# Kernel optimization log

Hardware: AMD Instinct MI355X
Metric: run time of the kernel (lower is better)

The kernel has to match this reference:

```python
import jax, jax.numpy as jnp
import numpy as np

HIDDEN = 2048
HEADS = 16
HEAD_DIM = HIDDEN // HEADS  # 128
ROPE_BASE = 10000.0
RMS_EPS = 1e-6
MINUS_INF = -10000.0


def rms_norm(x, w):
    xf = x.astype(jnp.float32)
    var = jnp.mean(xf * xf, axis=-1, keepdims=True)
    return w * (x * jax.lax.rsqrt(var + RMS_EPS))


def rotate_half(x):
    x1, x2 = jnp.split(x, 2, axis=-1)
    return jnp.concatenate((-x2, x1), axis=-1)


def rope_tables(seq_len, dtype):
    inv_freq = 1.0 / (ROPE_BASE ** (jnp.arange(0, HEAD_DIM, 2, dtype=jnp.float32) / HEAD_DIM))
    t = jnp.arange(seq_len, dtype=jnp.float32)
    freqs = jnp.einsum('i,j->ij', t, inv_freq)           # [S, D/2]
    emb = jnp.concatenate((freqs, freqs), axis=-1)       # [S, D]
    return jnp.cos(emb).astype(dtype), jnp.sin(emb).astype(dtype)


def setup_inputs() -> dict:
    key = jax.random.key(0)
    ks = jax.random.split(key, 6)
    B, S, H = 2, 2048, HIDDEN
    x = jax.random.normal(ks[0], (B, S, H), dtype=jnp.float32) * 0.5
    norm_w = jnp.ones((H,), dtype=jnp.float32)
    scale = 0.02
    wq = jax.random.normal(ks[1], (H, H), dtype=jnp.float32) * scale
    wk = jax.random.normal(ks[2], (H, H), dtype=jnp.float32) * scale
    wv = jax.random.normal(ks[3], (H, H), dtype=jnp.float32) * scale
    wo = jax.random.normal(ks[4], (H, H), dtype=jnp.float32) * scale
    position_ids = jnp.broadcast_to(jnp.arange(S, dtype=jnp.int32), (B, S))
    return {"x": x, "norm_w": norm_w, "wq": wq, "wk": wk, "wv": wv,
            "wo": wo, "position_ids": position_ids}


def reference(x, norm_w, wq, wk, wv, wo, position_ids):
    B, S, H = x.shape
    h = rms_norm(x, norm_w)
    # torch Linear: y = h @ W.T, weight is [out, in]
    def proj(w):
        return jnp.einsum('bsd,od->bso', h, w).reshape(B, S, HEADS, HEAD_DIM).transpose(0, 2, 1, 3)
    q, k, v = proj(wq), proj(wk), proj(wv)  # [B, Hh, S, D]
    cos, sin = rope_tables(S, x.dtype)
    cos = cos[position_ids][:, None]  # [B, 1, S, D]
    sin = sin[position_ids][:, None]
    q = q * cos + rotate_half(q) * sin
    k = k * cos + rotate_half(k) * sin
    scores = jnp.einsum('bhqd,bhkd->bhqk', q, k) / jnp.sqrt(jnp.float32(HEAD_DIM))
    causal = jnp.tril(jnp.ones((S, S), dtype=bool))
    scores = scores + jnp.where(causal, 0.0, MINUS_INF).astype(scores.dtype)
    probs = jax.nn.softmax(scores, axis=-1)
    ctx = jnp.einsum('bhqk,bhkd->bhqd', probs, v)          # [B, Hh, S, D]
    ctx = ctx.transpose(0, 2, 1, 3).reshape(B, S, H)
    out = jnp.einsum('bsd,od->bso', ctx, wo)
    return out
```

## Files before the change

### kernel.cpp

```cpp
#include <hip/hip_runtime.h>
#include <hip/hip_bf16.h>
#include <stdint.h>

#define S_LEN   2048
#define BATCH   2
#define HID     2048
#define NHEADS  16
#define HDIM    128
#define ROWS    (BATCH * S_LEN)
#define QKS     4096
#define ATT_SCALE 0.08838834764831843f
#define LOG2E     1.4426950408889634f

typedef __attribute__((ext_vector_type(8))) short s16x8;
typedef __attribute__((ext_vector_type(4))) float f32x4;

#define GLL16(gp, lp)                                                          \
  __builtin_amdgcn_global_load_lds(                                            \
      (__attribute__((address_space(1))) void*)(gp),                           \
      (__attribute__((address_space(3))) void*)(lp), 16, 0, 0)

__device__ __forceinline__ float bf2f(unsigned short u) {
  union { unsigned int i; float f; } v; v.i = ((unsigned int)u) << 16; return v.f;
}
__device__ __forceinline__ unsigned short f2bf(float f) {
  union { float f; unsigned int i; } v; v.f = f;
  unsigned int i = v.i;
  return (unsigned short)((i + 0x7FFFu + ((i >> 16) & 1u)) >> 16);
}
__device__ __forceinline__ void store_out(unsigned short* p, float v) { *p = f2bf(v); }
__device__ __forceinline__ void store_out(float* p, float v) { *p = v; }

__global__ __launch_bounds__(256) void cast4_kernel(const float* __restrict__ w0,
                                                    const float* __restrict__ w1,
                                                    const float* __restrict__ w2,
                                                    const float* __restrict__ w3,
                                                    unsigned short* __restrict__ dqkv,
                                                    unsigned short* __restrict__ dwo) {
  const int which = blockIdx.y;
  const float* src = (which == 0) ? w0 : (which == 1) ? w1 : (which == 2) ? w2 : w3;
  unsigned short* dst = (which < 3) ? dqkv + (size_t)which * HID * HID : dwo;
  int i = blockIdx.x * 256 + threadIdx.x;
  float4 v = ((const float4*)src)[i];
  ushort4 o;
  o.x = f2bf(v.x); o.y = f2bf(v.y); o.z = f2bf(v.z); o.w = f2bf(v.w);
  ((ushort4*)dst)[i] = o;
}

__global__ __launch_bounds__(256) void rmsnorm_kernel(const float* __restrict__ x,
                                                      const float* __restrict__ w,
                                                      unsigned short* __restrict__ h) {
  int row = blockIdx.x;
  int t = threadIdx.x;
  const float4* xr4 = (const float4*)(x + (size_t)row * HID);
  float4 a = xr4[t], b = xr4[t + 256];
  float ss = a.x*a.x + a.y*a.y + a.z*a.z + a.w*a.w
           + b.x*b.x + b.y*b.y + b.z*b.z + b.w*b.w;
#pragma unroll
  for (int off = 32; off >= 1; off >>= 1) ss += __shfl_xor(ss, off, 64);
  __shared__ float red[4];
  if ((t & 63) == 0) red[t >> 6] = ss;
  __syncthreads();
  float tot = red[0] + red[1] + red[2] + red[3];
  float rs = rsqrtf(tot * (1.0f / (float)HID) + 1e-6f);
  const float4* w4 = (const float4*)w;
  float4 wa = w4[t], wb = w4[t + 256];
  ushort4 oa, ob;
  oa.x = f2bf(a.x * wa.x * rs); oa.y = f2bf(a.y * wa.y * rs);
  oa.z = f2bf(a.z * wa.z * rs); oa.w = f2bf(a.w * wa.w * rs);
  ob.x = f2bf(b.x * wb.x * rs); ob.y = f2bf(b.y * wb.y * rs);
  ob.z = f2bf(b.z * wb.z * rs); ob.w = f2bf(b.w * wb.w * rs);
  ushort4* hr = (ushort4*)(h + (size_t)row * HID);
  hr[t] = oa; hr[t + 256] = ob;
}

__global__ void rope_tab_kernel(float* __restrict__ cost, float* __restrict__ sint) {
  int s = blockIdx.x, j = threadIdx.x;
  float inv = powf(10000.0f, -((float)j) / 64.0f);
  float ang = (float)s * inv;
  cost[s * 64 + j] = cosf(ang);
  sint[s * 64 + j] = sinf(ang);
}

__global__ __launch_bounds__(256) void rope_kernel(const int* __restrict__ pos_ids,
                                                   const float* __restrict__ cost,
                                                   const float* __restrict__ sint,
                                                   unsigned short* __restrict__ qk) {
  int row = blockIdx.x;
  int p = pos_ids[row];
  int t = threadIdx.x;
  int head = t >> 4;
  int j0 = (t & 15) * 4;
  size_t base = (size_t)row * QKS + head * HDIM;
  float4 c = *(const float4*)(cost + p * 64 + j0);
  float4 s = *(const float4*)(sint + p * 64 + j0);
#pragma unroll
  for (int which = 0; which < 2; which++) {
    unsigned short* ptr = qk + base + which * HID;
    float sc = which ? 1.0f : (ATT_SCALE * LOG2E);
    ushort4 v1 = *(ushort4*)(ptr + j0);
    ushort4 v2 = *(ushort4*)(ptr + 64 + j0);
    ushort4 o1, o2;
    o1.x = f2bf((bf2f(v1.x) * c.x - bf2f(v2.x) * s.x) * sc);
    o1.y = f2bf((bf2f(v1.y) * c.y - bf2f(v2.y) * s.y) * sc);
    o1.z = f2bf((bf2f(v1.z) * c.z - bf2f(v2.z) * s.z) * sc);
    o1.w = f2bf((bf2f(v1.w) * c.w - bf2f(v2.w) * s.w) * sc);
    o2.x = f2bf((bf2f(v2.x) * c.x + bf2f(v1.x) * s.x) * sc);
    o2.y = f2bf((bf2f(v2.y) * c.y + bf2f(v1.y) * s.y) * sc);
    o2.z = f2bf((bf2f(v2.z) * c.z + bf2f(v1.z) * s.z) * sc);
    o2.w = f2bf((bf2f(v2.w) * c.w + bf2f(v1.w) * s.w) * sc);
    *(ushort4*)(ptr + j0) = o1;
    *(ushort4*)(ptr + 64 + j0) = o2;
  }
}

#define SH(kt, bi, kk2) {                                                      \
    const unsigned short* sa_ = aQ + (size_t)(kt) * 64 + (kk2) * 32;           \
    const unsigned short* sb_ = bQ + (size_t)(kt) * 64 + (kk2) * 32;           \
    char* da_ = qsm + ((bi) * 2 + (kk2)) * 32768 + tid * 16;                   \
    GLL16(sa_, da_);                                                           \
    GLL16(sa_ + (size_t)128 * K, da_ + 8192);                                  \
    GLL16(sb_, da_ + 16384);                                                   \
    GLL16(sb_ + (size_t)128 * K, da_ + 16384 + 8192);                          \
  }

__global__ __launch_bounds__(512, 2) void gemm_qk_kernel(const unsigned short* __restrict__ A,
                                                         const unsigned short* __restrict__ B,
                                                         unsigned short* __restrict__ C,
                                                         int K, int N) {
  __shared__ __align__(16) unsigned short Qsm[2][2][2][256 * 32];
  const int bm = blockIdx.y, bn = blockIdx.x;
  const int tid = threadIdx.x;
  const int w = tid >> 6, wr = w >> 2, wc = w & 3;
  const int l = tid & 63, g = l >> 4, r = l & 15;
  const int KT = K >> 6;

  const int srow = tid >> 2;
  const int sg = (tid & 3) ^ ((tid >> 2) & 3) ^ ((tid >> 4) & 3);
  const unsigned short* aQ = A + (size_t)(bm * 256 + srow) * K + sg * 8;
  const unsigned short* bQ = B + (size_t)(bn * 256 + srow) * K + sg * 8;
  char* const qsm = (char*)Qsm;

  f32x4 zero = {0.f, 0.f, 0.f, 0.f};
  f32x4 acc[8][4];
#pragma unroll
  for (int mi = 0; mi < 8; mi++)
#pragma unroll
    for (int ni = 0; ni < 4; ni++) acc[mi][ni] = zero;

  const int ro = ((g ^ (r & 3) ^ ((r >> 2) & 3)) << 4);
  const int aOff = (wr * 128 + r) * 64 + ro;
  const int bOff = 16384 + (wc * 64 + r) * 64 + ro;

  SH(0, 0, 0); SH(0, 0, 1);

  for (int kt = 0; kt < KT; ++kt) {
    const int buf = kt & 1;
    const bool more = (kt + 1 < KT);
    const char* l0 = qsm + (buf * 2 + 0) * 32768;
    const char* l1 = qsm + (buf * 2 + 1) * 32768;

    asm volatile("s_waitcnt vmcnt(4)" ::: "memory");
    __builtin_amdgcn_s_barrier();
    __builtin_amdgcn_sched_barrier(0);
    s16x8 a[4], b[4];
#pragma unroll
    for (int ni = 0; ni < 4; ni++) b[ni] = *(const s16x8*)(l0 + bOff + ni * 1024);
#pragma unroll
    for (int i = 0; i < 4; i++) a[i] = *(const s16x8*)(l0 + aOff + i * 1024);
    if (more) SH(kt + 1, buf ^ 1, 0);
    __builtin_amdgcn_s_setprio(1);
#pragma unroll
    for (int ni = 0; ni < 4; ni++)
#pragma unroll
      for (int i = 0; i < 4; i++)
        acc[i][ni] = __builtin_amdgcn_mfma_f32_16x16x32_bf16(a[i], b[ni], acc[i][ni], 0, 0, 0);
    __builtin_amdgcn_s_setprio(0);

    s16x8 a2[4];
#pragma unroll
    for (int i = 0; i < 4; i++) a2[i] = *(const s16x8*)(l0 + aOff + (4 + i) * 1024);
    __builtin_amdgcn_s_setprio(1);
#pragma unroll
    for (int ni = 0; ni < 4; ni++)
#pragma unroll
      for (int i = 0; i < 4; i++)
        acc[4 + i][ni] = __builtin_amdgcn_mfma_f32_16x16x32_bf16(a2[i], b[ni], acc[4 + i][ni], 0, 0, 0);
    __builtin_amdgcn_s_setprio(0);

    if (more) { asm volatile("s_waitcnt vmcnt(4)" ::: "memory"); }
    else      { asm volatile("s_waitcnt vmcnt(0)" ::: "memory"); }
    __builtin_amdgcn_s_barrier();
    __builtin_amdgcn_sched_barrier(0);
#pragma unroll
    for (int ni = 0; ni < 4; ni++) b[ni] = *(const s16x8*)(l1 + bOff + ni * 1024);
#pragma unroll
    for (int i = 0; i < 4; i++) a[i] = *(const s16x8*)(l1 + aOff + i * 1024);
    if (more) SH(kt + 1, buf ^ 1, 1);
    __builtin_amdgcn_s_setprio(1);
#pragma unroll
    for (int ni = 0; ni < 4; ni++)
#pragma unroll
      for (int i = 0; i < 4; i++)
        acc[i][ni] = __builtin_amdgcn_mfma_f32_16x16x32_bf16(a[i], b[ni], acc[i][ni], 0, 0, 0);
    __builtin_amdgcn_s_setprio(0);

#pragma unroll
    for (int i = 0; i < 4; i++) a2[i] = *(const s16x8*)(l1 + aOff + (4 + i) * 1024);
    __builtin_amdgcn_s_setprio(1);
#pragma unroll
    for (int ni = 0; ni < 4; ni++)
#pragma unroll
      for (int i = 0; i < 4; i++)
        acc[4 + i][ni] = __builtin_amdgcn_mfma_f32_16x16x32_bf16(a2[i], b[ni], acc[4 + i][ni], 0, 0, 0);
    __builtin_amdgcn_s_setprio(0);
  }

#pragma unroll
  for (int mi = 0; mi < 8; mi++)
#pragma unroll
    for (int ni = 0; ni < 4; ni++) {
      const int crow = bm * 256 + wr * 128 + mi * 16 + g * 4;
      const int ccol = bn * 256 + wc * 64 + ni * 16 + r;
#pragma unroll
      for (int j = 0; j < 4; j++)
        store_out(&C[(size_t)(crow + j) * N + ccol], acc[mi][ni][j]);
    }
}
#undef SH

#define SA(kt, bi) {                                                           \
    const unsigned short* s_ = aS + (size_t)(kt) * 64;                         \
    char* d_ = (char*)Ab[bi] + tid * 16;                                       \
    GLL16(s_, d_);                                                             \
    GLL16(s_ + (size_t)64 * K, d_ + 8192);                                     \
  }
#define SB(kt, bi, hf) {                                                       \
    const unsigned short* s_ = bS + (size_t)(hf) * 128 * K + (size_t)(kt) * 64;\
    char* d_ = (char*)Bb[bi] + (hf) * 16384 + tid * 16;                        \
    GLL16(s_, d_);                                                             \
    GLL16(s_ + (size_t)64 * K, d_ + 8192);                                     \
  }

template <typename OutT, int NI, bool VT_OUT>
__global__ __launch_bounds__(512, 1) void gemm8_kernel(const unsigned short* __restrict__ A,
                                                       const unsigned short* __restrict__ B,
                                                       OutT* __restrict__ C, int K, int N) {
  __shared__ __align__(16) unsigned short Ab[3][128 * 64];
  __shared__ __align__(16) unsigned short Bb[3][NI * 64 * 64];
  const int bm = blockIdx.y, bn = blockIdx.x;
  const int tid = threadIdx.x;
  const int w = tid >> 6, wr = w >> 2, wc = w & 3;
  const int l = tid & 63, g = l >> 4, r = l & 15;
  const int KT = K >> 6;

  const int srow = tid >> 3;
  const int sgr = (tid & 7) ^ (srow & 7);
  const unsigned short* aS = A + (size_t)(bm * 128 + srow) * K + sgr * 8;
  const unsigned short* bS = B + (size_t)(bn * (NI * 64) + srow) * K + sgr * 8;

  f32x4 zero = {0.f, 0.f, 0.f, 0.f};
  f32x4 acc[4][NI];
#pragma unroll
  for (int mi = 0; mi < 4; mi++)
#pragma unroll
    for (int ni = 0; ni < NI; ni++) acc[mi][ni] = zero;

  const int swx = (r & 7) << 4;
  const int ks0 = (g << 4) ^ swx;
  const int ks1 = ((4 | g) << 4) ^ swx;
  const int aOff = (wr * 64 + r) * 128;
  const int bOff = (wc * (NI * 16) + r) * 128;

  SA(0, 0); SB(0, 0, 0); if (NI == 4) SB(0, 0, 1);
  SA(1, 1); SB(1, 1, 0); if (NI == 4) SB(1, 1, 1);

  int cur = 0;
  for (int kt = 0; kt < KT; ++kt) {
    const int b2 = (cur >= 1) ? cur - 1 : cur + 2;
    if (kt == KT - 1)      { asm volatile("s_waitcnt vmcnt(0)" ::: "memory"); }
    else if (NI == 4)      { asm volatile("s_waitcnt vmcnt(6)" ::: "memory"); }
    else                   { asm volatile("s_waitcnt vmcnt(4)" ::: "memory"); }
    __builtin_amdgcn_s_barrier();
    __builtin_amdgcn_sched_barrier(0);
    const char* lA = (const char*)Ab[cur];
    const char* lB = (const char*)Bb[cur];
    const bool more = (kt + 2 < KT);

    s16x8 a[4][2], b[NI][2];
#pragma unroll
    for (int mi = 0; mi < 4; mi++) {
      a[mi][0] = *(const s16x8*)(lA + aOff + mi * 2048 + ks0);
      a[mi][1] = *(const s16x8*)(lA + aOff + mi * 2048 + ks1);
    }
#pragma unroll
    for (int ni = 0; ni < NI / 2; ni++) {
      b[ni][0] = *(const s16x8*)(lB + bOff + ni * 2048 + ks0);
      b[ni][1] = *(const s16x8*)(lB + bOff + ni * 2048 + ks1);
    }
    if (more) { SA(kt + 2, b2); if (NI == 4) SB(kt + 2, b2, 0); }
    __builtin_amdgcn_s_setprio(1);
#pragma unroll
    for (int kk = 0; kk < 2; kk++)
#pragma unroll
      for (int ni = 0; ni < NI / 2; ni++)
#pragma unroll
        for (int mi = 0; mi < 4; mi++)
          acc[mi][ni] = __builtin_amdgcn_mfma_f32_16x16x32_bf16(a[mi][kk], b[ni][kk], acc[mi][ni], 0, 0, 0);
    __builtin_amdgcn_s_setprio(0);
    __builtin_amdgcn_sched_barrier(0);

#pragma unroll
    for (int ni = NI / 2; ni < NI; ni++) {
      b[ni][0] = *(const s16x8*)(lB + bOff + ni * 2048 + ks0);
      b[ni][1] = *(const s16x8*)(lB + bOff + ni * 2048 + ks1);
    }
    if (more) { if (NI == 4) { SB(kt + 2, b2, 1); } else { SB(kt + 2, b2, 0); } }
    __builtin_amdgcn_s_setprio(1);
#pragma unroll
    for (int kk = 0; kk < 2; kk++)
#pragma unroll
      for (int ni = NI / 2; ni < NI; ni++)
#pragma unroll
        for (int mi = 0; mi < 4; mi++)
          acc[mi][ni] = __builtin_amdgcn_mfma_f32_16x16x32_bf16(a[mi][kk], b[ni][kk], acc[mi][ni], 0, 0, 0);
    __builtin_amdgcn_s_setprio(0);
    cur = (cur == 2) ? 0 : cur + 1;
  }

#pragma unroll
  for (int mi = 0; mi < 4; mi++)
#pragma unroll
    for (int ni = 0; ni < NI; ni++) {
      const int crow = bm * 128 + wr * 64 + mi * 16 + g * 4;
      const int ccol = bn * (NI * 64) + wc * (NI * 16) + ni * 16 + r;
      if constexpr (VT_OUT) {
        const int bidx = crow >> 11;
        const int s0 = crow & (S_LEN - 1);
        const int vrow = (bidx * 16 + (ccol >> 7)) * 128 + (ccol & 127);
        ushort4 o;
        o.x = f2bf(acc[mi][ni][0]); o.y = f2bf(acc[mi][ni][1]);
        o.z = f2bf(acc[mi][ni][2]); o.w = f2bf(acc[mi][ni][3]);
        *(ushort4*)((unsigned short*)C + (size_t)vrow * S_LEN + s0) = o;
      } else {
#pragma unroll
        for (int j = 0; j < 4; j++)
          store_out(&C[(size_t)(crow + j) * N + ccol], acc[mi][ni][j]);
      }
    }
}

__global__ __launch_bounds__(256, 2) void attn_kernel(const unsigned short* __restrict__ QK,
                                                      const unsigned short* __restrict__ VT,
                                                      unsigned short* __restrict__ O) {
  __shared__ __align__(16) unsigned short Ksm[2][64 * 128];
  __shared__ __align__(16) unsigned short VTsm[2][128 * 64];
  __shared__ __align__(16) unsigned short Psm[4 * 16 * 64];
  const int bid = blockIdx.x;
  const int grp = bid & 7, idx = bid >> 3;
  const int qt = 31 - (idx >> 2);
  const int bh = (grp << 2) | (idx & 3);
  const int b = bh >> 4, hd = bh & 15;
  const int tid = threadIdx.x, w = tid >> 6, l = tid & 63, g = l >> 4, r = l & 15;
  const int qbs = qt * 64 + w * 16;

  const unsigned short* qp = QK + (size_t)(b * S_LEN + qbs + r) * QKS + hd * HDIM;
  s16x8 qf[4];
#pragma unroll
  for (int ks = 0; ks < 4; ks++) qf[ks] = *(const s16x8*)(qp + ks * 32 + g * 8);

  float mreg = -1e30f, lreg = 0.f;
  f32x4 zero = {0.f, 0.f, 0.f, 0.f};
  f32x4 oacc[8];
#pragma unroll
  for (int di = 0; di < 8; di++) oacc[di] = zero;

  const int cK = tid & 15, rowK = tid >> 4;
  const unsigned short* kp_base = QK + (size_t)(b * S_LEN + rowK) * QKS + HID + hd * HDIM
                                  + ((cK ^ (rowK & 7)) << 3);
  const int cV = tid & 7, dV = tid >> 3;
  const unsigned short* vp_base = VT + (size_t)(bh * 128 + dV) * S_LEN + ((cV ^ (dV & 7)) << 3);
  char* const ksm0 = (char*)Ksm;
  char* const vtsm0 = (char*)VTsm;
  char* const psm_w = (char*)Psm + w * 2048;
  const int pswz = (r & 7) << 4;

#define STAGE(kt, bufi)                                                        \
  {                                                                            \
    const unsigned short* kp_ = kp_base + (size_t)((kt) * 64) * QKS;           \
    const unsigned short* vp_ = vp_base + (kt) * 64;                           \
    char* kd_ = ksm0 + (bufi) * 16384;                                         \
    char* vd_ = vtsm0 + (bufi) * 16384;                                        \
    GLL16(kp_,                      kd_ + tid * 16);                           \
    GLL16(kp_ + (size_t)16 * QKS,   kd_ + (tid + 256) * 16);                   \
    GLL16(kp_ + (size_t)32 * QKS,   kd_ + (tid + 512) * 16);                   \
    GLL16(kp_ + (size_t)48 * QKS,   kd_ + (tid + 768) * 16);                   \
    GLL16(vp_,                      vd_ + tid * 16);                           \
    GLL16(vp_ + (size_t)32 * S_LEN, vd_ + (tid + 256) * 16);                   \
    GLL16(vp_ + (size_t)64 * S_LEN, vd_ + (tid + 512) * 16);                   \
    GLL16(vp_ + (size_t)96 * S_LEN, vd_ + (tid + 768) * 16);                   \
  }

  const int nt = qt + 1;
  STAGE(0, 0);

  for (int kt2 = 0; kt2 < nt; kt2++) {
    const int buf = kt2 & 1;
    asm volatile("s_waitcnt vmcnt(0)" ::: "memory");
    __builtin_amdgcn_s_barrier();
    __builtin_amdgcn_sched_barrier(0);
    if (kt2 + 1 < nt) STAGE(kt2 + 1, buf ^ 1);

    const char* ksm_c = ksm0 + buf * 16384;
    const char* vtsm_c = vtsm0 + buf * 16384;

    f32x4 sacc[4];
#pragma unroll
    for (int ni = 0; ni < 4; ni++) sacc[ni] = zero;
#pragma unroll
    for (int ni = 0; ni < 4; ni++) {
      const int krow = ni * 16 + r;
      const int swz = (krow & 7) << 4;
      const char* kb2 = ksm_c + krow * 256;
#pragma unroll
      for (int ks = 0; ks < 4; ks++) {
        s16x8 kf = *(const s16x8*)(kb2 + ((ks * 64 + g * 16) ^ swz));
        sacc[ni] = __builtin_amdgcn_mfma_f32_16x16x32_bf16(kf, qf[ks], sacc[ni], 0, 0, 0);
      }
    }

    if (kt2 == qt) {
#pragma unroll
      for (int ni = 0; ni < 4; ni++)
#pragma unroll
        for (int jj = 0; jj < 4; jj++)
          if ((kt2 * 64 + ni * 16 + g * 4 + jj) > (qbs + r)) sacc[ni][jj] = -1e30f;
    }

    float m0 = fmaxf(fmaxf(sacc[0][0], sacc[0][1]), fmaxf(sacc[0][2], sacc[0][3]));
    float m1 = fmaxf(fmaxf(sacc[1][0], sacc[1][1]), fmaxf(sacc[1][2], sacc[1][3]));
    float m2 = fmaxf(fmaxf(sacc[2][0], sacc[2][1]), fmaxf(sacc[2][2], sacc[2][3]));
    float m3 = fmaxf(fmaxf(sacc[3][0], sacc[3][1]), fmaxf(sacc[3][2], sacc[3][3]));
    float mx = fmaxf(fmaxf(m0, m1), fmaxf(m2, m3));
    mx = fmaxf(mx, __shfl_xor(mx, 16, 64));
    mx = fmaxf(mx, __shfl_xor(mx, 32, 64));

    if (__any(mx > mreg + 8.0f)) {
      float mn = fmaxf(mreg, mx);
      float corr = exp2f(mreg - mn);
      mreg = mn;
      lreg *= corr;
#pragma unroll
      for (int di = 0; di < 8; di++) oacc[di] = oacc[di] * corr;
    }

#pragma unroll
    for (int ni = 0; ni < 4; ni++)
#pragma unroll
      for (int jj = 0; jj < 4; jj++) sacc[ni][jj] = exp2f(sacc[ni][jj] - mreg);
    float s0 = (sacc[0][0] + sacc[0][1]) + (sacc[0][2] + sacc[0][3]);
    float s1 = (sacc[1][0] + sacc[1][1]) + (sacc[1][2] + sacc[1][3]);
    float s2 = (sacc[2][0] + sacc[2][1]) + (sacc[2][2] + sacc[2][3]);
    float s3 = (sacc[3][0] + sacc[3][1]) + (sacc[3][2] + sacc[3][3]);
    float sm = (s0 + s1) + (s2 + s3);
    sm += __shfl_xor(sm, 16, 64);
    sm += __shfl_xor(sm, 32, 64);
    lreg += sm;

#pragma unroll
    for (int ni = 0; ni < 4; ni++) {
      unsigned int pk01, pk23;
      asm("v_cvt_pk_bf16_f32 %0, %1, %2" : "=v"(pk01) : "v"(sacc[ni][0]), "v"(sacc[ni][1]));
      asm("v_cvt_pk_bf16_f32 %0, %1, %2" : "=v"(pk23) : "v"(sacc[ni][2]), "v"(sacc[ni][3]));
      const int byte0 = (r * 128 + ni * 32 + g * 8) ^ pswz;
      *(unsigned int*)(psm_w + byte0) = pk01;
      *(unsigned int*)(psm_w + byte0 + 4) = pk23;
    }

#pragma unroll
    for (int ksl = 0; ksl < 2; ksl++) {
      s16x8 pb = *(const s16x8*)(psm_w + ((r * 128 + ksl * 64 + g * 16) ^ pswz));
      const int kgran = ksl * 4 + g;
#pragma unroll
      for (int di = 0; di < 8; di++) {
        const int d = di * 16 + r;
        s16x8 vf = *(const s16x8*)(vtsm_c + d * 128 + ((kgran ^ (d & 7)) << 4));
        oacc[di] = __builtin_amdgcn_mfma_f32_16x16x32_bf16(vf, pb, oacc[di], 0, 0, 0);
      }
    }
  }
#undef STAGE

  const float inv = 1.0f / lreg;
  unsigned short* orow = O + (size_t)(b * S_LEN + qbs + r) * HID + hd * HDIM;
#pragma unroll
  for (int di = 0; di < 8; di++) {
    ushort4 o;
    o.x = f2bf(oacc[di][0] * inv); o.y = f2bf(oacc[di][1] * inv);
    o.z = f2bf(oacc[di][2] * inv); o.w = f2bf(oacc[di][3] * inv);
    *(ushort4*)(orow + di * 16 + g * 4) = o;
  }
}

extern "C" void kernel_launch(void* const* d_in, const int* in_sizes, int n_in,
                              void* d_out, int out_size, void* d_ws, size_t ws_size,
                              hipStream_t stream) {
  const float* x      = (const float*)d_in[0];
  const float* norm_w = (const float*)d_in[1];
  const float* wq     = (const float*)d_in[2];
  const float* wk     = (const float*)d_in[3];
  const float* wv     = (const float*)d_in[4];
  const float* wo     = (const float*)d_in[5];
  const int*   pos    = (const int*)d_in[6];
  float* out = (float*)d_out;

  char* ws = (char*)d_ws;
  const size_t WQKV_B = (size_t)3 * HID * HID * 2;
  const size_t WO_B   = (size_t)HID * HID * 2;
  const size_t H_B    = (size_t)ROWS * HID * 2;
  const size_t QK_B   = (size_t)ROWS * QKS * 2;

  unsigned short* wqkvb = (unsigned short*)(ws);
  unsigned short* vt    = (unsigned short*)(ws);
  unsigned short* wob   = (unsigned short*)(ws + WQKV_B);
  unsigned short* h     = (unsigned short*)(ws + WQKV_B + WO_B);
  unsigned short* qk    = (unsigned short*)(ws + WQKV_B + WO_B + H_B);
  float* cost = (float*)(ws + WQKV_B + WO_B + H_B + QK_B);
  float* sint = cost + (size_t)S_LEN * 64;

  dim3 cgrid(HID * HID / 4 / 256, 4);
  cast4_kernel<<<cgrid, 256, 0, stream>>>(wq, wk, wv, wo, wqkvb, wob);
  rope_tab_kernel<<<S_LEN, 64, 0, stream>>>(cost, sint);
  rmsnorm_kernel<<<ROWS, 256, 0, stream>>>(x, norm_w, h);

  dim3 qkgrid(2 * HID / 256, ROWS / 256);
  gemm_qk_kernel<<<qkgrid, 512, 0, stream>>>(h, wqkvb, qk, HID, QKS);

  dim3 vgrid(HID / 256, ROWS / 128);
  gemm8_kernel<unsigned short, 4, true><<<vgrid, 512, 0, stream>>>(
      h, wqkvb + (size_t)2 * HID * HID, vt, HID, S_LEN);

  rope_kernel<<<ROWS, 256, 0, stream>>>(pos, cost, sint, qk);

  attn_kernel<<<1024, 256, 0, stream>>>(qk, vt, h );

  dim3 ogrid(HID / 256, ROWS / 128);
  gemm8_kernel<float, 4, false><<<ogrid, 512, 0, stream>>>(h, wob, out, HID, HID);
}
```

Baseline: 256.2 us.

## Shrink attention KV tile to 32 keys and raise occupancy to four blocks

The attention kernel now processes 32-key tiles instead of 64, which halves its K, V and P shared-memory buffers and lets launch bounds request four blocks per CU instead of two. Swizzles, staging loads, the causal mask and the loop count are adjusted to match. The query-tile order across blocks is also changed to an interleaved pattern, to balance the causal workload across concurrently resident blocks. In exchange, there are twice as many barriers and softmax reductions per key, and less MFMA work per synchronization.

```diff
diff --git a/kernel.cpp b/kernel.cpp
--- a/kernel.cpp
+++ b/kernel.cpp
@@ -350,15 +350,16 @@
     }
 }
 
-__global__ __launch_bounds__(256, 2) void attn_kernel(const unsigned short* __restrict__ QK,
+__global__ __launch_bounds__(256, 4) void attn_kernel(const unsigned short* __restrict__ QK,
                                                       const unsigned short* __restrict__ VT,
                                                       unsigned short* __restrict__ O) {
-  __shared__ __align__(16) unsigned short Ksm[2][64 * 128];
-  __shared__ __align__(16) unsigned short VTsm[2][128 * 64];
-  __shared__ __align__(16) unsigned short Psm[4 * 16 * 64];
+  __shared__ __align__(16) unsigned short Ksm[2][32 * 128];
+  __shared__ __align__(16) unsigned short VTsm[2][128 * 32];
+  __shared__ __align__(16) unsigned short Psm[4 * 16 * 32];
   const int bid = blockIdx.x;
   const int grp = bid & 7, idx = bid >> 3;
-  const int qt = 31 - (idx >> 2);
+  const int m = idx >> 2, m4 = m & 7, seg = m >> 3;
+  const int qt = (seg == 0) ? 31 - m4 : (seg == 1) ? m4 : (seg == 2) ? 23 - m4 : 8 + m4;
   const int bh = (grp << 2) | (idx & 3);
   const int b = bh >> 4, hd = bh & 15;
   const int tid = threadIdx.x, w = tid >> 6, l = tid & 63, g = l >> 4, r = l & 15;
@@ -378,30 +379,26 @@
   const int cK = tid & 15, rowK = tid >> 4;
   const unsigned short* kp_base = QK + (size_t)(b * S_LEN + rowK) * QKS + HID + hd * HDIM
                                   + ((cK ^ (rowK & 7)) << 3);
-  const int cV = tid & 7, dV = tid >> 3;
-  const unsigned short* vp_base = VT + (size_t)(bh * 128 + dV) * S_LEN + ((cV ^ (dV & 7)) << 3);
+  const int cV = tid & 3, dV = tid >> 2;
+  const unsigned short* vp_base = VT + (size_t)(bh * 128 + dV) * S_LEN + ((cV ^ (dV & 3)) << 3);
   char* const ksm0 = (char*)Ksm;
   char* const vtsm0 = (char*)VTsm;
-  char* const psm_w = (char*)Psm + w * 2048;
-  const int pswz = (r & 7) << 4;
+  char* const psm_w = (char*)Psm + w * 1024;
+  const int pswz = (r & 3) << 4;
 
 #define STAGE(kt, bufi)                                                        \
   {                                                                            \
-    const unsigned short* kp_ = kp_base + (size_t)((kt) * 64) * QKS;           \
-    const unsigned short* vp_ = vp_base + (kt) * 64;                           \
-    char* kd_ = ksm0 + (bufi) * 16384;                                         \
-    char* vd_ = vtsm0 + (bufi) * 16384;                                        \
+    const unsigned short* kp_ = kp_base + (size_t)((kt) * 32) * QKS;           \
+    const unsigned short* vp_ = vp_base + (kt) * 32;                           \
+    char* kd_ = ksm0 + (bufi) * 8192;                                          \
+    char* vd_ = vtsm0 + (bufi) * 8192;                                         \
     GLL16(kp_,                      kd_ + tid * 16);                           \
     GLL16(kp_ + (size_t)16 * QKS,   kd_ + (tid + 256) * 16);                   \
-    GLL16(kp_ + (size_t)32 * QKS,   kd_ + (tid + 512) * 16);                   \
-    GLL16(kp_ + (size_t)48 * QKS,   kd_ + (tid + 768) * 16);                   \
     GLL16(vp_,                      vd_ + tid * 16);                           \
-    GLL16(vp_ + (size_t)32 * S_LEN, vd_ + (tid + 256) * 16);                   \
-    GLL16(vp_ + (size_t)64 * S_LEN, vd_ + (tid + 512) * 16);                   \
-    GLL16(vp_ + (size_t)96 * S_LEN, vd_ + (tid + 768) * 16);                   \
-  }
-
-  const int nt = qt + 1;
+    GLL16(vp_ + (size_t)64 * S_LEN, vd_ + (tid + 256) * 16);                   \
+  }
+
+  const int nt = 2 * qt + 2;
   STAGE(0, 0);
 
   for (int kt2 = 0; kt2 < nt; kt2++) {
@@ -411,14 +408,14 @@
     __builtin_amdgcn_sched_barrier(0);
     if (kt2 + 1 < nt) STAGE(kt2 + 1, buf ^ 1);
 
-    const char* ksm_c = ksm0 + buf * 16384;
-    const char* vtsm_c = vtsm0 + buf * 16384;
-
-    f32x4 sacc[4];
-#pragma unroll
-    for (int ni = 0; ni < 4; ni++) sacc[ni] = zero;
-#pragma unroll
-    for (int ni = 0; ni < 4; ni++) {
+    const char* ksm_c = ksm0 + buf * 8192;
+    const char* vtsm_c = vtsm0 + buf * 8192;
+
+    f32x4 sacc[2];
+#pragma unroll
+    for (int ni = 0; ni < 2; ni++) sacc[ni] = zero;
+#pragma unroll
+    for (int ni = 0; ni < 2; ni++) {
       const int krow = ni * 16 + r;
       const int swz = (krow & 7) << 4;
       const char* kb2 = ksm_c + krow * 256;
@@ -429,19 +426,17 @@
       }
     }
 
-    if (kt2 == qt) {
-#pragma unroll
-      for (int ni = 0; ni < 4; ni++)
+    if ((kt2 >> 1) == qt) {
+#pragma unroll
+      for (int ni = 0; ni < 2; ni++)
 #pragma unroll
         for (int jj = 0; jj < 4; jj++)
-          if ((kt2 * 64 + ni * 16 + g * 4 + jj) > (qbs + r)) sacc[ni][jj] = -1e30f;
+          if ((kt2 * 32 + ni * 16 + g * 4 + jj) > (qbs + r)) sacc[ni][jj] = -1e30f;
     }
 
     float m0 = fmaxf(fmaxf(sacc[0][0], sacc[0][1]), fmaxf(sacc[0][2], sacc[0][3]));
     float m1 = fmaxf(fmaxf(sacc[1][0], sacc[1][1]), fmaxf(sacc[1][2], sacc[1][3]));
-    float m2 = fmaxf(fmaxf(sacc[2][0], sacc[2][1]), fmaxf(sacc[2][2], sacc[2][3]));
-    float m3 = fmaxf(fmaxf(sacc[3][0], sacc[3][1]), fmaxf(sacc[3][2], sacc[3][3]));
-    float mx = fmaxf(fmaxf(m0, m1), fmaxf(m2, m3));
+    float mx = fmaxf(m0, m1);
     mx = fmaxf(mx, __shfl_xor(mx, 16, 64));
     mx = fmaxf(mx, __shfl_xor(mx, 32, 64));
 
@@ -455,38 +450,31 @@
     }
 
 #pragma unroll
-    for (int ni = 0; ni < 4; ni++)
+    for (int ni = 0; ni < 2; ni++)
 #pragma unroll
       for (int jj = 0; jj < 4; jj++) sacc[ni][jj] = exp2f(sacc[ni][jj] - mreg);
     float s0 = (sacc[0][0] + sacc[0][1]) + (sacc[0][2] + sacc[0][3]);
     float s1 = (sacc[1][0] + sacc[1][1]) + (sacc[1][2] + sacc[1][3]);
-    float s2 = (sacc[2][0] + sacc[2][1]) + (sacc[2][2] + sacc[2][3]);
-    float s3 = (sacc[3][0] + sacc[3][1]) + (sacc[3][2] + sacc[3][3]);
-    float sm = (s0 + s1) + (s2 + s3);
+    float sm = s0 + s1;
     sm += __shfl_xor(sm, 16, 64);
     sm += __shfl_xor(sm, 32, 64);
     lreg += sm;
 
 #pragma unroll
-    for (int ni = 0; ni < 4; ni++) {
+    for (int ni = 0; ni < 2; ni++) {
       unsigned int pk01, pk23;
       asm("v_cvt_pk_bf16_f32 %0, %1, %2" : "=v"(pk01) : "v"(sacc[ni][0]), "v"(sacc[ni][1]));
       asm("v_cvt_pk_bf16_f32 %0, %1, %2" : "=v"(pk23) : "v"(sacc[ni][2]), "v"(sacc[ni][3]));
-      const int byte0 = (r * 128 + ni * 32 + g * 8) ^ pswz;
-      *(unsigned int*)(psm_w + byte0) = pk01;
-      *(unsigned int*)(psm_w + byte0 + 4) = pk23;
-    }
-
-#pragma unroll
-    for (int ksl = 0; ksl < 2; ksl++) {
-      s16x8 pb = *(const s16x8*)(psm_w + ((r * 128 + ksl * 64 + g * 16) ^ pswz));
-      const int kgran = ksl * 4 + g;
-#pragma unroll
-      for (int di = 0; di < 8; di++) {
-        const int d = di * 16 + r;
-        s16x8 vf = *(const s16x8*)(vtsm_c + d * 128 + ((kgran ^ (d & 7)) << 4));
-        oacc[di] = __builtin_amdgcn_mfma_f32_16x16x32_bf16(vf, pb, oacc[di], 0, 0, 0);
-      }
+      uint2 pk; pk.x = pk01; pk.y = pk23;
+      *(uint2*)(psm_w + ((r * 64 + ni * 32 + g * 8) ^ pswz)) = pk;
+    }
+
+    s16x8 pb = *(const s16x8*)(psm_w + ((r * 64 + g * 16) ^ pswz));
+#pragma unroll
+    for (int di = 0; di < 8; di++) {
+      const int d = di * 16 + r;
+      s16x8 vf = *(const s16x8*)(vtsm_c + d * 64 + ((g ^ (d & 3)) << 4));
+      oacc[di] = __builtin_amdgcn_mfma_f32_16x16x32_bf16(vf, pb, oacc[di], 0, 0, 0);
     }
   }
 #undef STAGE
```

After: 272.1 us. +6.2%, slower.

## Enlarge attention query tile to 128 rows with two sub-tiles per wave

Applied to the files above, without the earlier changes.

Each attention block now covers 128 query rows, and each wave handles two 16-row sub-tiles that reuse every K fragment and V tile loaded into LDS. This halves the block count, cuts repeated K/V staging per query row, and changes the scheduling order to interleave long and short causal tiles. The row-sum reduction across lanes is deferred to the end. In exchange it doubles accumulator registers, which may reduce occupancy under launch_bounds(256,2), and waves idle on causal tiles past their rows.

```diff
diff --git a/kernel.cpp b/kernel.cpp
--- a/kernel.cpp
+++ b/kernel.cpp
@@ -358,22 +358,29 @@
   __shared__ __align__(16) unsigned short Psm[4 * 16 * 64];
   const int bid = blockIdx.x;
   const int grp = bid & 7, idx = bid >> 3;
-  const int qt = 31 - (idx >> 2);
+  const int m = idx >> 2;
+  const int qt = (m < 8) ? 15 - m : m - 8;
   const int bh = (grp << 2) | (idx & 3);
   const int b = bh >> 4, hd = bh & 15;
   const int tid = threadIdx.x, w = tid >> 6, l = tid & 63, g = l >> 4, r = l & 15;
-  const int qbs = qt * 64 + w * 16;
-
-  const unsigned short* qp = QK + (size_t)(b * S_LEN + qbs + r) * QKS + hd * HDIM;
-  s16x8 qf[4];
-#pragma unroll
-  for (int ks = 0; ks < 4; ks++) qf[ks] = *(const s16x8*)(qp + ks * 32 + g * 8);
-
-  float mreg = -1e30f, lreg = 0.f;
+  const int qbs = qt * 128 + w * 32;
+
+  s16x8 qf[2][4];
+#pragma unroll
+  for (int s = 0; s < 2; s++) {
+    const unsigned short* qp = QK + (size_t)(b * S_LEN + qbs + s * 16 + r) * QKS + hd * HDIM;
+#pragma unroll
+    for (int ks = 0; ks < 4; ks++) qf[s][ks] = *(const s16x8*)(qp + ks * 32 + g * 8);
+  }
+
+  float mreg[2] = {-1e30f, -1e30f};
+  float lregp[2] = {0.f, 0.f};
   f32x4 zero = {0.f, 0.f, 0.f, 0.f};
-  f32x4 oacc[8];
-#pragma unroll
-  for (int di = 0; di < 8; di++) oacc[di] = zero;
+  f32x4 oacc[2][8];
+#pragma unroll
+  for (int s = 0; s < 2; s++)
+#pragma unroll
+    for (int di = 0; di < 8; di++) oacc[s][di] = zero;
 
   const int cK = tid & 15, rowK = tid >> 4;
   const unsigned short* kp_base = QK + (size_t)(b * S_LEN + rowK) * QKS + HID + hd * HDIM
@@ -401,7 +408,7 @@
     GLL16(vp_ + (size_t)96 * S_LEN, vd_ + (tid + 768) * 16);                   \
   }
 
-  const int nt = qt + 1;
+  const int nt = 2 * qt + 2;
   STAGE(0, 0);
 
   for (int kt2 = 0; kt2 < nt; kt2++) {
@@ -411,94 +418,120 @@
     __builtin_amdgcn_sched_barrier(0);
     if (kt2 + 1 < nt) STAGE(kt2 + 1, buf ^ 1);
 
-    const char* ksm_c = ksm0 + buf * 16384;
-    const char* vtsm_c = vtsm0 + buf * 16384;
-
-    f32x4 sacc[4];
-#pragma unroll
-    for (int ni = 0; ni < 4; ni++) sacc[ni] = zero;
-#pragma unroll
-    for (int ni = 0; ni < 4; ni++) {
-      const int krow = ni * 16 + r;
-      const int swz = (krow & 7) << 4;
-      const char* kb2 = ksm_c + krow * 256;
-#pragma unroll
-      for (int ks = 0; ks < 4; ks++) {
-        s16x8 kf = *(const s16x8*)(kb2 + ((ks * 64 + g * 16) ^ swz));
-        sacc[ni] = __builtin_amdgcn_mfma_f32_16x16x32_bf16(kf, qf[ks], sacc[ni], 0, 0, 0);
-      }
-    }
-
-    if (kt2 == qt) {
-#pragma unroll
-      for (int ni = 0; ni < 4; ni++)
-#pragma unroll
-        for (int jj = 0; jj < 4; jj++)
-          if ((kt2 * 64 + ni * 16 + g * 4 + jj) > (qbs + r)) sacc[ni][jj] = -1e30f;
-    }
-
-    float m0 = fmaxf(fmaxf(sacc[0][0], sacc[0][1]), fmaxf(sacc[0][2], sacc[0][3]));
-    float m1 = fmaxf(fmaxf(sacc[1][0], sacc[1][1]), fmaxf(sacc[1][2], sacc[1][3]));
-    float m2 = fmaxf(fmaxf(sacc[2][0], sacc[2][1]), fmaxf(sacc[2][2], sacc[2][3]));
-    float m3 = fmaxf(fmaxf(sacc[3][0], sacc[3][1]), fmaxf(sacc[3][2], sacc[3][3]));
-    float mx = fmaxf(fmaxf(m0, m1), fmaxf(m2, m3));
-    mx = fmaxf(mx, __shfl_xor(mx, 16, 64));
-    mx = fmaxf(mx, __shfl_xor(mx, 32, 64));
-
-    if (__any(mx > mreg + 8.0f)) {
-      float mn = fmaxf(mreg, mx);
-      float corr = exp2f(mreg - mn);
-      mreg = mn;
-      lreg *= corr;
-#pragma unroll
-      for (int di = 0; di < 8; di++) oacc[di] = oacc[di] * corr;
-    }
-
-#pragma unroll
-    for (int ni = 0; ni < 4; ni++)
-#pragma unroll
-      for (int jj = 0; jj < 4; jj++) sacc[ni][jj] = exp2f(sacc[ni][jj] - mreg);
-    float s0 = (sacc[0][0] + sacc[0][1]) + (sacc[0][2] + sacc[0][3]);
-    float s1 = (sacc[1][0] + sacc[1][1]) + (sacc[1][2] + sacc[1][3]);
-    float s2 = (sacc[2][0] + sacc[2][1]) + (sacc[2][2] + sacc[2][3]);
-    float s3 = (sacc[3][0] + sacc[3][1]) + (sacc[3][2] + sacc[3][3]);
-    float sm = (s0 + s1) + (s2 + s3);
-    sm += __shfl_xor(sm, 16, 64);
-    sm += __shfl_xor(sm, 32, 64);
-    lreg += sm;
-
-#pragma unroll
-    for (int ni = 0; ni < 4; ni++) {
-      unsigned int pk01, pk23;
-      asm("v_cvt_pk_bf16_f32 %0, %1, %2" : "=v"(pk01) : "v"(sacc[ni][0]), "v"(sacc[ni][1]));
-      asm("v_cvt_pk_bf16_f32 %0, %1, %2" : "=v"(pk23) : "v"(sacc[ni][2]), "v"(sacc[ni][3]));
-      const int byte0 = (r * 128 + ni * 32 + g * 8) ^ pswz;
-      *(unsigned int*)(psm_w + byte0) = pk01;
-      *(unsigned int*)(psm_w + byte0 + 4) = pk23;
-    }
-
-#pragma unroll
-    for (int ksl = 0; ksl < 2; ksl++) {
-      s16x8 pb = *(const s16x8*)(psm_w + ((r * 128 + ksl * 64 + g * 16) ^ pswz));
-      const int kgran = ksl * 4 + g;
-#pragma unroll
-      for (int di = 0; di < 8; di++) {
-        const int d = di * 16 + r;
-        s16x8 vf = *(const s16x8*)(vtsm_c + d * 128 + ((kgran ^ (d & 7)) << 4));
-        oacc[di] = __builtin_amdgcn_mfma_f32_16x16x32_bf16(vf, pb, oacc[di], 0, 0, 0);
+    const bool active = (kt2 * 64) <= (qbs + 31);
+    if (active) {
+      const char* ksm_c = ksm0 + buf * 16384;
+      const char* vtsm_c = vtsm0 + buf * 16384;
+
+      f32x4 sacc[2][4];
+#pragma unroll
+      for (int s = 0; s < 2; s++)
+#pragma unroll
+        for (int ni = 0; ni < 4; ni++) sacc[s][ni] = zero;
+#pragma unroll
+      for (int ni = 0; ni < 4; ni++) {
+        const int krow = ni * 16 + r;
+        const int swz = (krow & 7) << 4;
+        const char* kb2 = ksm_c + krow * 256;
+#pragma unroll
+        for (int ks = 0; ks < 4; ks++) {
+          s16x8 kf = *(const s16x8*)(kb2 + ((ks * 64 + g * 16) ^ swz));
+#pragma unroll
+          for (int s = 0; s < 2; s++)
+            sacc[s][ni] = __builtin_amdgcn_mfma_f32_16x16x32_bf16(kf, qf[s][ks], sacc[s][ni], 0, 0, 0);
+        }
+      }
+
+#pragma unroll
+      for (int s = 0; s < 2; s++) {
+        if ((kt2 * 64 + 63) > (qbs + s * 16)) {
+#pragma unroll
+          for (int ni = 0; ni < 4; ni++)
+#pragma unroll
+            for (int jj = 0; jj < 4; jj++)
+              if ((kt2 * 64 + ni * 16 + g * 4 + jj) > (qbs + s * 16 + r)) sacc[s][ni][jj] = -1e30f;
+        }
+      }
+
+      float mx[2];
+#pragma unroll
+      for (int s = 0; s < 2; s++) {
+        float m0 = fmaxf(fmaxf(sacc[s][0][0], sacc[s][0][1]), fmaxf(sacc[s][0][2], sacc[s][0][3]));
+        float m1 = fmaxf(fmaxf(sacc[s][1][0], sacc[s][1][1]), fmaxf(sacc[s][1][2], sacc[s][1][3]));
+        float m2 = fmaxf(fmaxf(sacc[s][2][0], sacc[s][2][1]), fmaxf(sacc[s][2][2], sacc[s][2][3]));
+        float m3 = fmaxf(fmaxf(sacc[s][3][0], sacc[s][3][1]), fmaxf(sacc[s][3][2], sacc[s][3][3]));
+        float v = fmaxf(fmaxf(m0, m1), fmaxf(m2, m3));
+        v = fmaxf(v, __shfl_xor(v, 16, 64));
+        v = fmaxf(v, __shfl_xor(v, 32, 64));
+        mx[s] = v;
+      }
+
+      bool grow = (mx[0] > mreg[0] + 8.0f) || (mx[1] > mreg[1] + 8.0f);
+      if (__any(grow)) {
+#pragma unroll
+        for (int s = 0; s < 2; s++) {
+          float mn = fmaxf(mreg[s], mx[s]);
+          float corr = exp2f(mreg[s] - mn);
+          mreg[s] = mn;
+          lregp[s] *= corr;
+#pragma unroll
+          for (int di = 0; di < 8; di++) oacc[s][di] = oacc[s][di] * corr;
+        }
+      }
+
+#pragma unroll
+      for (int s = 0; s < 2; s++) {
+#pragma unroll
+        for (int ni = 0; ni < 4; ni++)
+#pragma unroll
+          for (int jj = 0; jj < 4; jj++) sacc[s][ni][jj] = exp2f(sacc[s][ni][jj] - mreg[s]);
+        float s0 = (sacc[s][0][0] + sacc[s][0][1]) + (sacc[s][0][2] + sacc[s][0][3]);
+        float s1 = (sacc[s][1][0] + sacc[s][1][1]) + (sacc[s][1][2] + sacc[s][1][3]);
+        float s2 = (sacc[s][2][0] + sacc[s][2][1]) + (sacc[s][2][2] + sacc[s][2][3]);
+        float s3 = (sacc[s][3][0] + sacc[s][3][1]) + (sacc[s][3][2] + sacc[s][3][3]);
+        lregp[s] += (s0 + s1) + (s2 + s3);
+      }
+
+#pragma unroll
+      for (int s = 0; s < 2; s++) {
+#pragma unroll
+        for (int ni = 0; ni < 4; ni++) {
+          unsigned int pk01, pk23;
+          asm("v_cvt_pk_bf16_f32 %0, %1, %2" : "=v"(pk01) : "v"(sacc[s][ni][0]), "v"(sacc[s][ni][1]));
+          asm("v_cvt_pk_bf16_f32 %0, %1, %2" : "=v"(pk23) : "v"(sacc[s][ni][2]), "v"(sacc[s][ni][3]));
+          uint2 pk; pk.x = pk01; pk.y = pk23;
+          *(uint2*)(psm_w + ((r * 128 + ni * 32 + g * 8) ^ pswz)) = pk;
+        }
+#pragma unroll
+        for (int ksl = 0; ksl < 2; ksl++) {
+          s16x8 pb = *(const s16x8*)(psm_w + ((r * 128 + ksl * 64 + g * 16) ^ pswz));
+          const int kgran = ksl * 4 + g;
+#pragma unroll
+          for (int di = 0; di < 8; di++) {
+            const int d = di * 16 + r;
+            s16x8 vf = *(const s16x8*)(vtsm_c + d * 128 + ((kgran ^ (d & 7)) << 4));
+            oacc[s][di] = __builtin_amdgcn_mfma_f32_16x16x32_bf16(vf, pb, oacc[s][di], 0, 0, 0);
+          }
+        }
       }
     }
   }
 #undef STAGE
 
-  const float inv = 1.0f / lreg;
-  unsigned short* orow = O + (size_t)(b * S_LEN + qbs + r) * HID + hd * HDIM;
-#pragma unroll
-  for (int di = 0; di < 8; di++) {
-    ushort4 o;
-    o.x = f2bf(oacc[di][0] * inv); o.y = f2bf(oacc[di][1] * inv);
-    o.z = f2bf(oacc[di][2] * inv); o.w = f2bf(oacc[di][3] * inv);
-    *(ushort4*)(orow + di * 16 + g * 4) = o;
+#pragma unroll
+  for (int s = 0; s < 2; s++) {
+    float lsum = lregp[s];
+    lsum += __shfl_xor(lsum, 16, 64);
+    lsum += __shfl_xor(lsum, 32, 64);
+    const float inv = 1.0f / lsum;
+    unsigned short* orow = O + (size_t)(b * S_LEN + qbs + s * 16 + r) * HID + hd * HDIM;
+#pragma unroll
+    for (int di = 0; di < 8; di++) {
+      ushort4 o;
+      o.x = f2bf(oacc[s][di][0] * inv); o.y = f2bf(oacc[s][di][1] * inv);
+      o.z = f2bf(oacc[s][di][2] * inv); o.w = f2bf(oacc[s][di][3] * inv);
+      *(ushort4*)(orow + di * 16 + g * 4) = o;
+    }
   }
 }
 
@@ -542,7 +575,7 @@
 
   rope_kernel<<<ROWS, 256, 0, stream>>>(pos, cost, sint, qk);
 
-  attn_kernel<<<1024, 256, 0, stream>>>(qk, vt, h );
+  attn_kernel<<<512, 256, 0, stream>>>(qk, vt, h );
 
   dim3 ogrid(HID / 256, ROWS / 128);
   gemm8_kernel<float, 4, false><<<ogrid, 512, 0, stream>>>(h, wob, out, HID, HID);
```

New measurement: 263.3 us. 2.8% more time.
